# Performance work log

Measured on AMD Instinct MI355X. Metric: run time of the kernel, lower is better.

## Reference

```python
import jax, jax.numpy as jnp
import numpy as np

HEADS = 16
HEAD_DIM = 1024 // HEADS  # 64
SCALE = float(np.sqrt(HEAD_DIM))  # math.sqrt(features // heads)


def setup_inputs() -> dict:
    key = jax.random.key(0)
    ks = jax.random.split(key, 6)
    n, m, d, c = 2048, 2048, 1024, 768
    return {
        "x": jax.random.normal(ks[0], (n, d), dtype=jnp.float32),
        "ctx": jax.random.normal(ks[1], (m, c), dtype=jnp.float32),
        "Wq": jax.random.normal(ks[2], (d, d), dtype=jnp.float32) * (1.0 / np.sqrt(d)),
        "Wk": jax.random.normal(ks[3], (c, d), dtype=jnp.float32) * (1.0 / np.sqrt(c)),
        "Wv": jax.random.normal(ks[4], (c, d), dtype=jnp.float32) * (1.0 / np.sqrt(c)),
        "Wo": jax.random.normal(ks[5], (d, d), dtype=jnp.float32) * (1.0 / np.sqrt(d)),
    }


def reference(x, ctx, Wq, Wk, Wv, Wo):
    n, d = x.shape
    q = (x @ Wq).reshape(n, HEADS, HEAD_DIM).transpose(1, 0, 2)      # h n d
    k = (ctx @ Wk).reshape(-1, HEADS, HEAD_DIM).transpose(1, 0, 2)   # h m d
    v = (ctx @ Wv).reshape(-1, HEADS, HEAD_DIM).transpose(1, 0, 2)   # h m d
    scores = jnp.einsum("hnd,hmd->hnm", q, k) / SCALE
    attn = jax.nn.softmax(scores, axis=-1)
    out = jnp.einsum("hnm,hmd->hnd", attn, v)                        # h n d
    out = out.transpose(1, 0, 2).reshape(n, d)                       # n (h d)
    return out @ Wo
```

## Files before the change

kernel.cpp:

```cpp
#include <hip/hip_runtime.h>
#include <hip/hip_bf16.h>
#include <stdint.h>

typedef unsigned short bfu;
typedef __attribute__((ext_vector_type(8))) short short8;
typedef __attribute__((ext_vector_type(4))) float f32x4;

__device__ __forceinline__ bfu f2bf(float f) {
  union { float f; uint32_t u; } v; v.f = f;
  uint32_t r = (v.u + 0x7fffu + ((v.u >> 16) & 1u)) >> 16;
  return (bfu)r;
}

__device__ __forceinline__ void gload16(const void* g, void* l) {
  __builtin_amdgcn_global_load_lds((const __attribute__((address_space(1))) void*)g,
                                   (__attribute__((address_space(3))) void*)l, 16, 0, 0);
}

__device__ __forceinline__ void conv_body(const float* __restrict__ in, bfu* __restrict__ out,
                                          int i) {
  const float4* p = (const float4*)in + (size_t)i * 2;
  float4 a = p[0], b = p[1];
  union { bfu h[8]; uint4 v; } o;
  o.h[0] = f2bf(a.x); o.h[1] = f2bf(a.y); o.h[2] = f2bf(a.z); o.h[3] = f2bf(a.w);
  o.h[4] = f2bf(b.x); o.h[5] = f2bf(b.y); o.h[6] = f2bf(b.z); o.h[7] = f2bf(b.w);
  ((uint4*)out)[i] = o.v;
}

__device__ __forceinline__ void trans_body(const float* __restrict__ W, bfu* __restrict__ WT,
                                           int Kd, int n0, int k0) {
  __shared__ float tile[32][33];
  const int tx = threadIdx.x & 31, ty = threadIdx.x >> 5;
#pragma unroll
  for (int i = 0; i < 32; i += 8)
    tile[ty + i][tx] = W[(size_t)(k0 + ty + i) * 1024 + n0 + tx];
  __syncthreads();
#pragma unroll
  for (int i = 0; i < 32; i += 8)
    WT[(size_t)(n0 + ty + i) * Kd + k0 + tx] = f2bf(tile[tx][ty + i]);
}

__global__ __launch_bounds__(256) void prep_kernel(
    const float* __restrict__ x, const float* __restrict__ ctx,
    const float* __restrict__ Wq, const float* __restrict__ Wk,
    const float* __restrict__ Wv, const float* __restrict__ Wo,
    bfu* xb, bfu* ctxb, bfu* WTq, bfu* WTk, bfu* WTv, bfu* WTo) {
  int b = blockIdx.x;
  if (b < 1024)       conv_body(x, xb, b * 256 + threadIdx.x);
  else if (b < 1792)  conv_body(ctx, ctxb, (b - 1024) * 256 + threadIdx.x);
  else if (b < 2816) { b -= 1792; trans_body(Wq, WTq, 1024, (b & 31) * 32, (b >> 5) * 32); }
  else if (b < 3584) { b -= 2816; trans_body(Wk, WTk, 768, (b & 31) * 32, (b >> 5) * 32); }
  else if (b < 4352) { b -= 3584; trans_body(Wv, WTv, 768, (b & 31) * 32, (b >> 5) * 32); }
  else               { b -= 4352; trans_body(Wo, WTo, 1024, (b & 31) * 32, (b >> 5) * 32); }
}

typedef bfu AsArr[2][4][128][8];
typedef bfu BsArr[2][4][64][8];

__device__ __forceinline__ void gemm_body(AsArr& As2, BsArr& Bs2,
    const bfu* __restrict__ A, const bfu* __restrict__ BT,
    bfu* __restrict__ Cb, float* __restrict__ Cf,
    int N, int K, float scale, int m0, int n0) {
  const int tid = threadIdx.x, lane = tid & 63, wave = tid >> 6;
  const int g = lane >> 4, c = lane & 15;
  const int wm = wave * 32;
  const int nt = K / 32;

  auto stage = [&](int buf, int kt) {
#pragma unroll
    for (int u = 0; u < 3; ++u) {
      int idx = wave * 3 + u;
      if (idx < 8) {
        int g2 = idx & 3, rb = idx >> 2;
        gload16(&A[(size_t)(m0 + rb * 64 + lane) * K + kt + g2 * 8], &As2[buf][g2][rb * 64][0]);
      } else {
        int g2 = idx - 8;
        gload16(&BT[(size_t)(n0 + lane) * K + kt + g2 * 8], &Bs2[buf][g2][0][0]);
      }
    }
  };

  f32x4 acc[2][4] = {};
  stage(0, 0);
  for (int t = 0; t < nt; ++t) {
    __syncthreads();
    if (t + 1 < nt) stage((t + 1) & 1, (t + 1) * 32);
    const int b = t & 1;
    short8 af[2], bfr[4];
#pragma unroll
    for (int i = 0; i < 2; ++i) af[i] = *(const short8*)&As2[b][g][wm + i * 16 + c][0];
#pragma unroll
    for (int j = 0; j < 4; ++j) bfr[j] = *(const short8*)&Bs2[b][g][j * 16 + c][0];
#pragma unroll
    for (int i = 0; i < 2; ++i)
#pragma unroll
      for (int j = 0; j < 4; ++j)
        acc[i][j] = __builtin_amdgcn_mfma_f32_16x16x32_bf16(af[i], bfr[j], acc[i][j], 0, 0, 0);
  }
#pragma unroll
  for (int i = 0; i < 2; ++i)
#pragma unroll
    for (int j = 0; j < 4; ++j) {
      int row = m0 + wm + i * 16 + g * 4;
      int col = n0 + j * 16 + c;
#pragma unroll
      for (int r = 0; r < 4; ++r) {
        float v = acc[i][j][r] * scale;
        if (Cb) Cb[(size_t)(row + r) * N + col] = f2bf(v);
        else    Cf[(size_t)(row + r) * N + col] = v;
      }
    }
}

__global__ __launch_bounds__(256) void gemm3_kernel(
    const bfu* __restrict__ xb, const bfu* __restrict__ WTq, bfu* __restrict__ Qb,
    const bfu* __restrict__ ctxb, const bfu* __restrict__ WTk, bfu* __restrict__ Kb,
    const bfu* __restrict__ WTv, bfu* __restrict__ Vtb) {
  __shared__ alignas(16) bfu As2[2][4][128][8];
  __shared__ alignas(16) bfu Bs2[2][4][64][8];
  int bid = blockIdx.x, p = bid >> 8, r = bid & 255;
  if (p == 0)
    gemm_body(As2, Bs2, xb, WTq, Qb, nullptr, 1024, 1024, 0.125f, (r >> 4) * 128, (r & 15) * 64);
  else if (p == 1)
    gemm_body(As2, Bs2, ctxb, WTk, Kb, nullptr, 1024, 768, 1.0f, (r >> 4) * 128, (r & 15) * 64);
  else
    gemm_body(As2, Bs2, WTv, ctxb, Vtb, nullptr, 2048, 768, 1.0f, (r >> 5) * 128, (r & 31) * 64);
}

__global__ __launch_bounds__(256) void gemmo_kernel(const bfu* __restrict__ AO,
                                                    const bfu* __restrict__ WTo,
                                                    float* __restrict__ out) {
  __shared__ alignas(16) bfu As2[2][4][128][8];
  __shared__ alignas(16) bfu Bs2[2][4][64][8];
  int bid = blockIdx.x;
  gemm_body(As2, Bs2, AO, WTo, nullptr, out, 1024, 1024, 1.0f, (bid >> 4) * 128, (bid & 15) * 64);
}

__global__ __launch_bounds__(256) void attn_kernel(
    const bfu* __restrict__ Q, const bfu* __restrict__ Kmat,
    const bfu* __restrict__ Vt, bfu* __restrict__ O) {
  __shared__ alignas(16) bfu Ks[3][8][64][8];
  __shared__ alignas(16) bfu Vs[3][8][64][8];
  __shared__ alignas(16) bfu Ps[2][64][72];
  const int tid = threadIdx.x, wave = tid >> 6, lane = tid & 63;
  const int g = lane >> 4, c = lane & 15;
  const int h = blockIdx.y;
  const int qblk = blockIdx.x * 64;
  const int col0 = h * 64;

  short8 qf[4][2];
#pragma unroll
  for (int qt = 0; qt < 4; ++qt) {
    qf[qt][0] = *(const short8*)&Q[(size_t)(qblk + qt * 16 + c) * 1024 + col0 + g * 8];
    qf[qt][1] = *(const short8*)&Q[(size_t)(qblk + qt * 16 + c) * 1024 + col0 + 32 + g * 8];
  }

  short8 ones;
#pragma unroll
  for (int e = 0; e < 8; ++e) ones[e] = (short)0x3F80;

  f32x4 o_acc[4] = {};
  f32x4 lacc = {};

  auto stage = [&](int buf, int kv0) {
#pragma unroll
    for (int u = 0; u < 4; ++u) {
      int idx = wave * 4 + u;
      if (idx < 8)
        gload16(&Kmat[(size_t)(kv0 + lane) * 1024 + col0 + idx * 8], &Ks[buf][idx][0][0]);
      else
        gload16(&Vt[(size_t)(col0 + lane) * 2048 + kv0 + (idx - 8) * 8], &Vs[buf][idx - 8][0][0]);
    }
  };

  auto qk_exp = [&](int bQ, int pb) {
    short8 kf0 = *(const short8*)&Ks[bQ][g][wave * 16 + c][0];
    short8 kf1 = *(const short8*)&Ks[bQ][4 + g][wave * 16 + c][0];
    f32x4 s[4] = {};
    __builtin_amdgcn_s_setprio(1);
#pragma unroll
    for (int qt = 0; qt < 4; ++qt) {
      s[qt] = __builtin_amdgcn_mfma_f32_16x16x32_bf16(qf[qt][0], kf0, s[qt], 0, 0, 0);
      s[qt] = __builtin_amdgcn_mfma_f32_16x16x32_bf16(qf[qt][1], kf1, s[qt], 0, 0, 0);
    }
    __builtin_amdgcn_s_setprio(0);
#pragma unroll
    for (int qt = 0; qt < 4; ++qt)
#pragma unroll
      for (int j = 0; j < 4; ++j)
        Ps[pb][qt * 16 + g * 4 + j][wave * 16 + c] = f2bf(__expf(s[qt][j]));
  };

  auto pv = [&](int pb, int vb) {
    __builtin_amdgcn_s_setprio(1);
#pragma unroll
    for (int kc = 0; kc < 2; ++kc) {
      short8 pf = *(const short8*)&Ps[pb][wave * 16 + c][kc * 32 + g * 8];
      lacc = __builtin_amdgcn_mfma_f32_16x16x32_bf16(pf, ones, lacc, 0, 0, 0);
#pragma unroll
      for (int fd = 0; fd < 4; ++fd) {
        short8 vf = *(const short8*)&Vs[vb][kc * 4 + g][fd * 16 + c][0];
        o_acc[fd] = __builtin_amdgcn_mfma_f32_16x16x32_bf16(pf, vf, o_acc[fd], 0, 0, 0);
      }
    }
    __builtin_amdgcn_s_setprio(0);
  };

  stage(0, 0);
  __syncthreads();
  stage(1, 64);
  qk_exp(0, 0);
  __syncthreads();
  for (int t = 1; t < 32; ++t) {
    stage((t + 1) % 3, ((t + 1) & 31) * 64);
    qk_exp(t % 3, t & 1);
    pv((t - 1) & 1, (t - 1) % 3);
    __syncthreads();
  }
  pv(1, 1);

  const int q0 = qblk + wave * 16;
#pragma unroll
  for (int fd = 0; fd < 4; ++fd)
#pragma unroll
    for (int j = 0; j < 4; ++j) {
      float v = o_acc[fd][j] / lacc[j];
      O[(size_t)(q0 + g * 4 + j) * 1024 + col0 + fd * 16 + c] = f2bf(v);
    }
}

extern "C" void kernel_launch(void* const* d_in, const int* in_sizes, int n_in,
                              void* d_out, int out_size, void* d_ws, size_t ws_size,
                              hipStream_t stream) {
  const float* x   = (const float*)d_in[0];
  const float* ctx = (const float*)d_in[1];
  const float* Wq  = (const float*)d_in[2];
  const float* Wk  = (const float*)d_in[3];
  const float* Wv  = (const float*)d_in[4];
  const float* Wo  = (const float*)d_in[5];
  float* out = (float*)d_out;

  bfu* ws   = (bfu*)d_ws;
  bfu* xb   = ws;
  bfu* WTk  = xb + 2048 * 1024;
  bfu* WTv  = WTk + 1024 * 768;
  bfu* WTo  = WTv + 1024 * 768;
  bfu* Qb   = WTo + 1024 * 1024;
  bfu* Kb   = Qb + 2048 * 1024;
  bfu* Vtb  = Kb + 2048 * 1024;
  bfu* WTq  = (bfu*)d_out;
  bfu* ctxb = WTq + 1024 * 1024;

  dim3 blk(256);
  prep_kernel<<<5376, blk, 0, stream>>>(x, ctx, Wq, Wk, Wv, Wo, xb, ctxb, WTq, WTk, WTv, WTo);
  gemm3_kernel<<<768, blk, 0, stream>>>(xb, WTq, Qb, ctxb, WTk, Kb, WTv, Vtb);
  attn_kernel<<<dim3(32, 16), blk, 0, stream>>>(Qb, Kb, Vtb, xb);
  gemmo_kernel<<<256, blk, 0, stream>>>(xb, WTo, out);
}
```

Baseline: 115.3 us.

## Use 128x128 tiles for QKV projections and fold log2e into Q scale

Replaces the QKV projection GEMM's 128x64 tiles with 128x128 tiles, each wave computing a 64x64 sub-tile, which halves the block count to 384. The aim is more data reuse per LDS load and fewer global loads per output element. It also folds log2(e) into the Q scaling so attention can use exp2f instead of __expf. The trade-offs are higher register pressure from 16 accumulators per wave and fewer blocks than CUs to fill the GPU.

```diff
diff --git a/kernel.cpp b/kernel.cpp
--- a/kernel.cpp
+++ b/kernel.cpp
@@ -5,6 +5,8 @@
 typedef unsigned short bfu;
 typedef __attribute__((ext_vector_type(8))) short short8;
 typedef __attribute__((ext_vector_type(4))) float f32x4;
+
+#define LOG2E 1.4426950408889634f
 
 __device__ __forceinline__ bfu f2bf(float f) {
   union { float f; uint32_t u; } v; v.f = f;
@@ -54,6 +56,78 @@
   else               { b -= 4352; trans_body(Wo, WTo, 1024, (b & 31) * 32, (b >> 5) * 32); }
 }
 
+typedef bfu Tile128[2][4][128][8];
+
+__device__ __forceinline__ void gemm128_body(Tile128& As2, Tile128& Bs2,
+    const bfu* __restrict__ A, const bfu* __restrict__ BT,
+    bfu* __restrict__ Cb, int N, int K, float scale, int m0, int n0) {
+  const int tid = threadIdx.x, lane = tid & 63, wave = tid >> 6;
+  const int g = lane >> 4, c = lane & 15;
+  const int wm = (wave >> 1) * 64, wn = (wave & 1) * 64;
+  const int nt = K / 32;
+
+  auto stage = [&](int buf, int kt) {
+#pragma unroll
+    for (int u = 0; u < 4; ++u) {
+      int idx = wave * 4 + u;
+      if (idx < 8) {
+        int kg = idx & 3, rb = idx >> 2;
+        gload16(&A[(size_t)(m0 + rb * 64 + lane) * K + kt + kg * 8], &As2[buf][kg][rb * 64][0]);
+      } else {
+        int kg = (idx - 8) & 3, rb = (idx - 8) >> 2;
+        gload16(&BT[(size_t)(n0 + rb * 64 + lane) * K + kt + kg * 8], &Bs2[buf][kg][rb * 64][0]);
+      }
+    }
+  };
+
+  f32x4 acc[4][4] = {};
+  stage(0, 0);
+  for (int t = 0; t < nt; ++t) {
+    __syncthreads();
+    if (t + 1 < nt) stage((t + 1) & 1, (t + 1) * 32);
+    const int b = t & 1;
+    short8 af[4], bfr[4];
+#pragma unroll
+    for (int i = 0; i < 4; ++i) {
+      af[i]  = *(const short8*)&As2[b][g][wm + i * 16 + c][0];
+      bfr[i] = *(const short8*)&Bs2[b][g][wn + i * 16 + c][0];
+    }
+#pragma unroll
+    for (int i = 0; i < 4; ++i)
+#pragma unroll
+      for (int j = 0; j < 4; ++j)
+        acc[i][j] = __builtin_amdgcn_mfma_f32_16x16x32_bf16(af[i], bfr[j], acc[i][j], 0, 0, 0);
+  }
+#pragma unroll
+  for (int i = 0; i < 4; ++i)
+#pragma unroll
+    for (int j = 0; j < 4; ++j) {
+      int row = m0 + wm + i * 16 + g * 4;
+      int col = n0 + wn + j * 16 + c;
+#pragma unroll
+      for (int r = 0; r < 4; ++r)
+        Cb[(size_t)(row + r) * N + col] = f2bf(acc[i][j][r] * scale);
+    }
+}
+
+__global__ __launch_bounds__(256) void gemm3_kernel(
+    const bfu* __restrict__ xb, const bfu* __restrict__ WTq, bfu* __restrict__ Qb,
+    const bfu* __restrict__ ctxb, const bfu* __restrict__ WTk, bfu* __restrict__ Kb,
+    const bfu* __restrict__ WTv, bfu* __restrict__ Vtb) {
+  __shared__ alignas(16) bfu As2[2][4][128][8];
+  __shared__ alignas(16) bfu Bs2[2][4][128][8];
+  int bid = blockIdx.x;
+  if (bid < 128)
+    gemm128_body(As2, Bs2, xb, WTq, Qb, 1024, 1024, 0.125f * LOG2E, (bid >> 3) * 128, (bid & 7) * 128);
+  else if (bid < 256) {
+    int r = bid - 128;
+    gemm128_body(As2, Bs2, ctxb, WTk, Kb, 1024, 768, 1.0f, (r >> 3) * 128, (r & 7) * 128);
+  } else {
+    int r = bid - 256;
+    gemm128_body(As2, Bs2, WTv, ctxb, Vtb, 2048, 768, 1.0f, (r >> 4) * 128, (r & 15) * 128);
+  }
+}
+
 typedef bfu AsArr[2][4][128][8];
 typedef bfu BsArr[2][4][64][8];
 
@@ -110,21 +184,6 @@
         else    Cf[(size_t)(row + r) * N + col] = v;
       }
     }
-}
-
-__global__ __launch_bounds__(256) void gemm3_kernel(
-    const bfu* __restrict__ xb, const bfu* __restrict__ WTq, bfu* __restrict__ Qb,
-    const bfu* __restrict__ ctxb, const bfu* __restrict__ WTk, bfu* __restrict__ Kb,
-    const bfu* __restrict__ WTv, bfu* __restrict__ Vtb) {
-  __shared__ alignas(16) bfu As2[2][4][128][8];
-  __shared__ alignas(16) bfu Bs2[2][4][64][8];
-  int bid = blockIdx.x, p = bid >> 8, r = bid & 255;
-  if (p == 0)
-    gemm_body(As2, Bs2, xb, WTq, Qb, nullptr, 1024, 1024, 0.125f, (r >> 4) * 128, (r & 15) * 64);
-  else if (p == 1)
-    gemm_body(As2, Bs2, ctxb, WTk, Kb, nullptr, 1024, 768, 1.0f, (r >> 4) * 128, (r & 15) * 64);
-  else
-    gemm_body(As2, Bs2, WTv, ctxb, Vtb, nullptr, 2048, 768, 1.0f, (r >> 5) * 128, (r & 31) * 64);
 }
 
 __global__ __launch_bounds__(256) void gemmo_kernel(const bfu* __restrict__ AO,
@@ -188,7 +247,7 @@
     for (int qt = 0; qt < 4; ++qt)
 #pragma unroll
       for (int j = 0; j < 4; ++j)
-        Ps[pb][qt * 16 + g * 4 + j][wave * 16 + c] = f2bf(__expf(s[qt][j]));
+        Ps[pb][qt * 16 + g * 4 + j][wave * 16 + c] = f2bf(exp2f(s[qt][j]));
   };
 
   auto pv = [&](int pb, int vb) {
@@ -253,7 +312,7 @@
 
   dim3 blk(256);
   prep_kernel<<<5376, blk, 0, stream>>>(x, ctx, Wq, Wk, Wv, Wo, xb, ctxb, WTq, WTk, WTv, WTo);
-  gemm3_kernel<<<768, blk, 0, stream>>>(xb, WTq, Qb, ctxb, WTk, Kb, WTv, Vtb);
+  gemm3_kernel<<<384, blk, 0, stream>>>(xb, WTq, Qb, ctxb, WTk, Kb, WTv, Vtb);
   attn_kernel<<<dim3(32, 16), blk, 0, stream>>>(Qb, Kb, Vtb, xb);
   gemmo_kernel<<<256, blk, 0, stream>>>(xb, WTo, out);
 }
```

Measured after the change: 116.1 us. About the same (+0.7%).
